# Optimization experiments

Measured on AMD Instinct MI355X. Metric: run time of the kernel, lower is better.

The kernel has to match this reference:

```python
import jax, jax.numpy as jnp
import numpy as np

N_NODES = 50000
N_EDGES = 1250000
IN_CH = 64
HID = 64
N_CLASSES = 10
N_GRAPHS = 128


def _xavier(key, shape):
    fan_out, fan_in = shape
    limit = np.sqrt(6.0 / (fan_in + fan_out))
    return jax.random.uniform(key, shape, jnp.float32, -limit, limit)


def setup_inputs() -> dict:
    key = jax.random.key(0)
    ks = jax.random.split(key, 12)
    x = jax.random.normal(ks[0], (N_NODES, IN_CH), jnp.float32)
    edge_index = jax.random.randint(ks[1], (2, N_EDGES), 0, N_NODES, jnp.int64)
    batch = jnp.sort(jax.random.randint(ks[2], (N_NODES,), 0, N_GRAPHS, jnp.int64))
    return {
        "x": x,
        "edge_index": edge_index,
        "batch": batch,
        # GraphConv i: lin_rel (weight+bias) applied to aggregated neighbors,
        # lin_root (no bias) applied to self features. Weights are [out, in].
        "W1_rel": _xavier(ks[3], (HID, IN_CH)), "b1": jnp.zeros((HID,), jnp.float32),
        "W1_root": _xavier(ks[4], (HID, IN_CH)),
        "W2_rel": _xavier(ks[5], (HID, HID)), "b2": jnp.zeros((HID,), jnp.float32),
        "W2_root": _xavier(ks[6], (HID, HID)),
        "W3_rel": _xavier(ks[7], (HID, HID)), "b3": jnp.zeros((HID,), jnp.float32),
        "W3_root": _xavier(ks[8], (HID, HID)),
        "W_lin": _xavier(ks[9], (N_CLASSES, HID)), "b_lin": jnp.zeros((N_CLASSES,), jnp.float32),
    }


def _graph_conv(x, src, dst, W_rel, b, W_root):
    # sum-aggregate neighbor features: gather at src, scatter-add at dst
    agg = jax.ops.segment_sum(x[src], dst, num_segments=N_NODES)  # [N, F]
    return agg @ W_rel.T + b + x @ W_root.T


def reference(x, edge_index, batch, W1_rel, b1, W1_root, W2_rel, b2, W2_root,
              W3_rel, b3, W3_root, W_lin, b_lin):
    src, dst = edge_index[0], edge_index[1]
    h = jax.nn.relu(_graph_conv(x, src, dst, W1_rel, b1, W1_root))
    h = jax.nn.relu(_graph_conv(h, src, dst, W2_rel, b2, W2_root))
    h = _graph_conv(h, src, dst, W3_rel, b3, W3_root)
    # global mean pool over graphs
    sums = jax.ops.segment_sum(h, batch, num_segments=N_GRAPHS)        # [G, HID]
    counts = jax.ops.segment_sum(jnp.ones((h.shape[0],), h.dtype), batch,
                                 num_segments=N_GRAPHS)
    pooled = sums / jnp.maximum(counts, 1.0)[:, None]
    out = pooled @ W_lin.T + b_lin  # dropout inactive in eval mode
    return (pooled, out)
```

## Files before the change

### kernel.cpp

```cpp
#include <hip/hip_runtime.h>

#define N_NODES   50000
#define HID       64
#define N_GRAPHS  128
#define N_CLASSES 10
#define NP        196
#define EPA       2048
#define PCAP      8192

typedef __attribute__((ext_vector_type(8))) short short8;
typedef __attribute__((ext_vector_type(4))) float f32x4;

__device__ __forceinline__ unsigned bf16rne(float f) {
    unsigned u = __float_as_uint(f);
    return (u + 0x7fffu + ((u >> 16) & 1u)) >> 16;
}
__device__ __forceinline__ unsigned pack_bf16x2(float lo, float hi) {
    return bf16rne(lo) | (bf16rne(hi) << 16);
}



__global__ void cvt_kernel(const float* __restrict__ x, unsigned short* __restrict__ xb,
                           int* __restrict__ gcursor) {
    if (blockIdx.x == 0 && threadIdx.x < NP) gcursor[threadIdx.x] = 0;
    int i = blockIdx.x * blockDim.x + threadIdx.x;
    if (i < N_NODES * 16) {
        float4 v = ((const float4*)x)[i];
        uint2 o;
        o.x = pack_bf16x2(v.x, v.y);
        o.y = pack_bf16x2(v.z, v.w);
        ((uint2*)xb)[i] = o;
    }
}


__global__ __launch_bounds__(256) void bucket_kernel(
    const int* __restrict__ src, const int* __restrict__ dst,
    int* __restrict__ gcursor, unsigned* __restrict__ packed, int E) {
    __shared__ int hist[NP], scp[NP], base[NP], cnt2[NP];
    __shared__ int sc[256];
    __shared__ unsigned stag[EPA];
    const int t = threadIdx.x;
    const int e0 = blockIdx.x * EPA;
    const int e1 = min(e0 + EPA, E);
    for (int i = t; i < NP; i += 256) { hist[i] = 0; cnt2[i] = 0; }
    __syncthreads();
    for (int e = e0 + t; e < e1; e += 256)
        atomicAdd(&hist[dst[e] >> 8], 1);
    __syncthreads();
    sc[t] = (t < NP) ? hist[t] : 0;
    __syncthreads();
    for (int off = 1; off < 256; off <<= 1) {
        int add = (t >= off) ? sc[t - off] : 0;
        __syncthreads();
        sc[t] += add;
        __syncthreads();
    }
    if (t < NP) {
        scp[t] = sc[t] - hist[t];
        if (hist[t] > 0) base[t] = atomicAdd(&gcursor[t], hist[t]);
    }
    __syncthreads();
    for (int e = e0 + t; e < e1; e += 256) {
        int d = dst[e], s = src[e];
        int p = d >> 8;
        int idx = scp[p] + atomicAdd(&cnt2[p], 1);
        stag[idx] = (unsigned)s | ((unsigned)(d & 255) << 16) | ((unsigned)p << 24);
    }
    __syncthreads();
    const int n = e1 - e0;
    for (int i = t; i < n; i += 256) {
        unsigned v = stag[i];
        int p = v >> 24;
        packed[(size_t)p * PCAP + base[p] + (i - scp[p])] = v & 0x00FFFFFFu;
    }
}

__global__ __launch_bounds__(256) void build_kernel(
    const unsigned* __restrict__ packed, const int* __restrict__ gcursor,
    int* __restrict__ offsets, unsigned short* __restrict__ csr,
    int* __restrict__ sums_zero) {
    __shared__ int hist[256], lofs[256], cnt[256], sc[256], gv[256];
    __shared__ unsigned short lcsr[PCAP];
    const int p = blockIdx.x, t = threadIdx.x;

    if (p == 0) {
        for (int i = t; i < N_GRAPHS * 64 + N_GRAPHS; i += 256) sums_zero[i] = 0;
    }

    int v = (t < NP) ? gcursor[t] : 0;
    sc[t] = v; gv[t] = v;
    __syncthreads();
    for (int off = 1; off < 256; off <<= 1) {
        int add = (t >= off) ? sc[t - off] : 0;
        __syncthreads();
        sc[t] += add;
        __syncthreads();
    }
    const int pb = sc[p] - gv[p];
    const int ne = gv[p];
    if (p == NP - 1 && t == 0) offsets[N_NODES] = sc[NP - 1];
    __syncthreads();

    const unsigned* mypk = packed + (size_t)p * PCAP;
    hist[t] = 0; cnt[t] = 0;
    __syncthreads();
    for (int i = t; i < ne; i += 256)
        atomicAdd(&hist[(mypk[i] >> 16) & 255], 1);
    __syncthreads();
    sc[t] = hist[t];
    __syncthreads();
    for (int off = 1; off < 256; off <<= 1) {
        int add = (t >= off) ? sc[t - off] : 0;
        __syncthreads();
        sc[t] += add;
        __syncthreads();
    }
    lofs[t] = sc[t] - hist[t];
    int node = p * 256 + t;
    if (node < N_NODES) offsets[node] = pb + lofs[t];
    __syncthreads();
    for (int i = t; i < ne; i += 256) {
        unsigned vv = mypk[i];
        int dl = (vv >> 16) & 255;
        int slot = lofs[dl] + atomicAdd(&cnt[dl], 1);
        lcsr[slot] = (unsigned short)(vv & 0xFFFFu);
    }
    __syncthreads();
    for (int i = t; i < ne; i += 256) csr[pb + i] = lcsr[i];
}


__global__ __launch_bounds__(256) void gather_kernel(
    const unsigned short* __restrict__ hin,
    const int* __restrict__ offsets, const unsigned short* __restrict__ csr_src,
    unsigned short* __restrict__ agg) {
    const int w = threadIdx.x >> 6, lane = threadIdx.x & 63;
    const int rg = lane >> 3;
    const int cg = lane & 7;
    const int n = blockIdx.x * 4 + w;
    const int beg = offsets[n], end = offsets[n + 1];

    float acc[8] = {0.f, 0.f, 0.f, 0.f, 0.f, 0.f, 0.f, 0.f};
    for (int base = beg; base < end; base += 64) {
        int cnt = min(64, end - base);
        int sidx = (base + lane < end) ? (int)csr_src[base + lane] : 0;
        for (int kb = 0; kb < cnt; kb += 32) {
            uint4 u[4];
#pragma unroll
            for (int p = 0; p < 4; ++p) {
                int e = kb + 8 * p + rg;
                int r = __shfl(sidx, e);
                if (e < cnt)
                    u[p] = *((const uint4*)(hin + (size_t)r * 64) + cg);
                else
                    u[p] = make_uint4(0u, 0u, 0u, 0u);
            }
#pragma unroll
            for (int p = 0; p < 4; ++p) {
                acc[0] += __uint_as_float(u[p].x << 16);
                acc[1] += __uint_as_float(u[p].x & 0xffff0000u);
                acc[2] += __uint_as_float(u[p].y << 16);
                acc[3] += __uint_as_float(u[p].y & 0xffff0000u);
                acc[4] += __uint_as_float(u[p].z << 16);
                acc[5] += __uint_as_float(u[p].z & 0xffff0000u);
                acc[6] += __uint_as_float(u[p].w << 16);
                acc[7] += __uint_as_float(u[p].w & 0xffff0000u);
            }
        }
    }
#pragma unroll
    for (int m = 8; m <= 32; m <<= 1)
#pragma unroll
        for (int j = 0; j < 8; ++j)
            acc[j] += __shfl_xor(acc[j], m);
    if (rg == 0) {
        uint4 o;
        o.x = pack_bf16x2(acc[0], acc[1]);
        o.y = pack_bf16x2(acc[2], acc[3]);
        o.z = pack_bf16x2(acc[4], acc[5]);
        o.w = pack_bf16x2(acc[6], acc[7]);
        *((uint4*)(agg + (size_t)n * 64) + cg) = o;
    }
}


template <int RELU>
__global__ __launch_bounds__(256) void linear_kernel(
    const unsigned short* __restrict__ agg,
    const unsigned short* __restrict__ hin,
    const float* __restrict__ Wrel, const float* __restrict__ bias,
    const float* __restrict__ Wroot, unsigned short* __restrict__ hout) {
    __shared__ unsigned short outT[4][16][72];

    const int tid = threadIdx.x;
    const int w = tid >> 6, lane = tid & 63;
    const int q = lane >> 4, c = lane & 15;
    const int g0 = (blockIdx.x * 4 + w) * 16;
    if (g0 >= N_NODES) return;

    short8 brel[4][2], broot[4][2];
    float biasv[4];
#pragma unroll
    for (int t = 0; t < 4; ++t) {
        int o = t * 16 + c;
        biasv[t] = bias[o];
#pragma unroll
        for (int s = 0; s < 2; ++s) {
            const float4* pr = (const float4*)(Wrel  + o * 64 + s * 32 + q * 8);
            const float4* po = (const float4*)(Wroot + o * 64 + s * 32 + q * 8);
            float4 r0 = pr[0], r1 = pr[1], z0 = po[0], z1 = po[1];
            short8 rr, zz;
            rr[0] = (short)bf16rne(r0.x); rr[1] = (short)bf16rne(r0.y);
            rr[2] = (short)bf16rne(r0.z); rr[3] = (short)bf16rne(r0.w);
            rr[4] = (short)bf16rne(r1.x); rr[5] = (short)bf16rne(r1.y);
            rr[6] = (short)bf16rne(r1.z); rr[7] = (short)bf16rne(r1.w);
            zz[0] = (short)bf16rne(z0.x); zz[1] = (short)bf16rne(z0.y);
            zz[2] = (short)bf16rne(z0.z); zz[3] = (short)bf16rne(z0.w);
            zz[4] = (short)bf16rne(z1.x); zz[5] = (short)bf16rne(z1.y);
            zz[6] = (short)bf16rne(z1.z); zz[7] = (short)bf16rne(z1.w);
            brel[t][s] = rr; broot[t][s] = zz;
        }
    }

    const int na = min(g0 + c, N_NODES - 1);
    short8 a_agg[2], a_x[2];
#pragma unroll
    for (int s = 0; s < 2; ++s) {
        a_agg[s] = *(const short8*)(agg + (size_t)na * 64 + s * 32 + q * 8);
        a_x[s]   = *(const short8*)(hin + (size_t)na * 64 + s * 32 + q * 8);
    }

    f32x4 acc4[4];
#pragma unroll
    for (int t = 0; t < 4; ++t) {
        f32x4 a0 = {biasv[t], biasv[t], biasv[t], biasv[t]};
        a0 = __builtin_amdgcn_mfma_f32_16x16x32_bf16(a_agg[0], brel[t][0], a0, 0, 0, 0);
        a0 = __builtin_amdgcn_mfma_f32_16x16x32_bf16(a_agg[1], brel[t][1], a0, 0, 0, 0);
        a0 = __builtin_amdgcn_mfma_f32_16x16x32_bf16(a_x[0],  broot[t][0], a0, 0, 0, 0);
        a0 = __builtin_amdgcn_mfma_f32_16x16x32_bf16(a_x[1],  broot[t][1], a0, 0, 0, 0);
        acc4[t] = a0;
    }

#pragma unroll
    for (int t = 0; t < 4; ++t)
#pragma unroll
        for (int r = 0; r < 4; ++r) {
            float v = acc4[t][r];
            if (RELU) v = fmaxf(v, 0.f);
            outT[w][q * 4 + r][t * 16 + c] = (unsigned short)bf16rne(v);
        }

#pragma unroll
    for (int it = 0; it < 2; ++it) {
        int row = it * 8 + (lane >> 3);
        int ch = (lane & 7) * 8;
        int n = g0 + row;
        if (n < N_NODES) {
            short8 v = *(const short8*)&outT[w][row][ch];
            *(short8*)(hout + (size_t)n * 64 + ch) = v;
        }
    }
}


__global__ __launch_bounds__(256) void pool_kernel(
    const unsigned short* __restrict__ h, const int* __restrict__ batch,
    float* __restrict__ sums, int* __restrict__ cnt) {
    int tid = threadIdx.x;
    int w = tid >> 6, lane = tid & 63;
    int n0 = blockIdx.x * 128 + w * 32;
    if (n0 >= N_NODES) return;
    int nend = min(n0 + 32, N_NODES);
    int cur = batch[n0];
    float acc = 0.f;
    int run = 0;
    for (int n = n0; n < nend; ++n) {
        int g = batch[n];
        if (g != cur) {
            atomicAdd(&sums[cur * 64 + lane], acc);
            if (lane == 0) atomicAdd(&cnt[cur], run);
            acc = 0.f; run = 0; cur = g;
        }
        unsigned u = h[(size_t)n * 64 + lane];
        acc += __uint_as_float(u << 16);
        run++;
    }
    atomicAdd(&sums[cur * 64 + lane], acc);
    if (lane == 0) atomicAdd(&cnt[cur], run);
}

__global__ void final_kernel(const float* __restrict__ sums, const int* __restrict__ cnt,
                             const float* __restrict__ Wlin, const float* __restrict__ blin,
                             float* __restrict__ out) {
    __shared__ float pl[64];
    int g = blockIdx.x, lane = threadIdx.x;
    float cdiv = fmaxf((float)cnt[g], 1.0f);
    float p = sums[g * 64 + lane] / cdiv;
    out[g * 64 + lane] = p;
    pl[lane] = p;
    __syncthreads();
    if (lane < N_CLASSES) {
        float o = blin[lane];
#pragma unroll
        for (int k = 0; k < 64; ++k) o += pl[k] * Wlin[lane * 64 + k];
        out[N_GRAPHS * 64 + g * N_CLASSES + lane] = o;
    }
}


extern "C" void kernel_launch(void* const* d_in, const int* in_sizes, int n_in,
                              void* d_out, int out_size, void* d_ws, size_t ws_size,
                              hipStream_t stream) {
    const float* x     = (const float*)d_in[0];
    const int*   ei    = (const int*)d_in[1];
    const int*   batch = (const int*)d_in[2];
    const float* W1r = (const float*)d_in[3];
    const float* b1  = (const float*)d_in[4];
    const float* W1o = (const float*)d_in[5];
    const float* W2r = (const float*)d_in[6];
    const float* b2  = (const float*)d_in[7];
    const float* W2o = (const float*)d_in[8];
    const float* W3r = (const float*)d_in[9];
    const float* b3  = (const float*)d_in[10];
    const float* W3o = (const float*)d_in[11];
    const float* Wl  = (const float*)d_in[12];
    const float* bl  = (const float*)d_in[13];
    float* out = (float*)d_out;

    const int E = in_sizes[1] / 2;
    const int* src = ei;
    const int* dst = ei + E;

    char* p = (char*)d_ws;
    unsigned short* xb  = (unsigned short*)p; p += (size_t)N_NODES * 64 * 2;
    unsigned short* h1  = (unsigned short*)p; p += (size_t)N_NODES * 64 * 2;
    unsigned short* h2  = (unsigned short*)p; p += (size_t)N_NODES * 64 * 2;
    unsigned short* agg = (unsigned short*)p; p += (size_t)N_NODES * 64 * 2;
    unsigned short* h3  = h1;
    unsigned* packed    = (unsigned*)p; p += (size_t)NP * PCAP * 4;
    unsigned short* csr = (unsigned short*)p; p += (size_t)E * 2;
    int* offsets   = (int*)p;   p += (size_t)(N_NODES + 1) * 4;
    int* gcursor   = (int*)p;   p += NP * 4;
    float* sums    = (float*)p; p += (size_t)N_GRAPHS * 64 * 4;
    int* cnt       = (int*)p;   p += N_GRAPHS * 4;

    const int NCHUNK = (E + EPA - 1) / EPA;
    cvt_kernel<<<(N_NODES * 16 + 255) / 256, 256, 0, stream>>>(x, xb, gcursor);
    bucket_kernel<<<NCHUNK, 256, 0, stream>>>(src, dst, gcursor, packed, E);
    build_kernel<<<NP, 256, 0, stream>>>(packed, gcursor, offsets, csr, (int*)sums);

    const int GB = N_NODES / 4;
    const int LB = (N_NODES + 63) / 64;
    gather_kernel<<<GB, 256, 0, stream>>>(xb, offsets, csr, agg);
    linear_kernel<1><<<LB, 256, 0, stream>>>(agg, xb, W1r, b1, W1o, h1);
    gather_kernel<<<GB, 256, 0, stream>>>(h1, offsets, csr, agg);
    linear_kernel<1><<<LB, 256, 0, stream>>>(agg, h1, W2r, b2, W2o, h2);
    gather_kernel<<<GB, 256, 0, stream>>>(h2, offsets, csr, agg);
    linear_kernel<0><<<LB, 256, 0, stream>>>(agg, h2, W3r, b3, W3o, h3);

    pool_kernel<<<(N_NODES + 127) / 128, 256, 0, stream>>>(h3, batch, sums, cnt);
    final_kernel<<<N_GRAPHS, 64, 0, stream>>>(sums, cnt, Wl, bl, out);
}
```

Measured before the change: 271.5 us.

## Replace two-level bucketed CSR build with global atomic count/scan/scatter

Swaps the bucket-then-local-sort CSR construction for a simpler pipeline: per-node degree counting with global atomics, a per-block scan to produce offsets and cursors, then a scatter using a global atomic on each destination's cursor. It drops the large packed staging buffer and the shared-memory local sort, but adds two full passes of global atomics over the edges. Edge order within each node becomes nondeterministic, so the order of floating-point sums in the gather can vary from run to run.

```diff
diff --git a/kernel.cpp b/kernel.cpp
--- a/kernel.cpp
+++ b/kernel.cpp
@@ -5,8 +5,7 @@
 #define N_GRAPHS  128
 #define N_CLASSES 10
 #define NP        196
-#define EPA       2048
-#define PCAP      8192
+#define NPAD      50176
 
 typedef __attribute__((ext_vector_type(8))) short short8;
 typedef __attribute__((ext_vector_type(4))) float f32x4;
@@ -20,11 +19,12 @@
 }
 
 
+#define NZERO (NPAD + N_GRAPHS * 64 + N_GRAPHS)
 
 __global__ void cvt_kernel(const float* __restrict__ x, unsigned short* __restrict__ xb,
-                           int* __restrict__ gcursor) {
-    if (blockIdx.x == 0 && threadIdx.x < NP) gcursor[threadIdx.x] = 0;
+                           int* __restrict__ zspan) {
     int i = blockIdx.x * blockDim.x + threadIdx.x;
+    if (i < NZERO) zspan[i] = 0;
     if (i < N_NODES * 16) {
         float4 v = ((const float4*)x)[i];
         uint2 o;
@@ -35,21 +35,32 @@
 }
 
 
-__global__ __launch_bounds__(256) void bucket_kernel(
-    const int* __restrict__ src, const int* __restrict__ dst,
-    int* __restrict__ gcursor, unsigned* __restrict__ packed, int E) {
-    __shared__ int hist[NP], scp[NP], base[NP], cnt2[NP];
+__global__ __launch_bounds__(256) void count_kernel(
+    const int* __restrict__ dst, int* __restrict__ deg, int E) {
+    int e = blockIdx.x * 256 + threadIdx.x;
+    if (e < E) atomicAdd(&deg[dst[e]], 1);
+}
+
+__global__ __launch_bounds__(256) void offsets_kernel(
+    const int* __restrict__ deg, int* __restrict__ offsets,
+    int* __restrict__ cursor) {
+    __shared__ int part[256];
     __shared__ int sc[256];
-    __shared__ unsigned stag[EPA];
-    const int t = threadIdx.x;
-    const int e0 = blockIdx.x * EPA;
-    const int e1 = min(e0 + EPA, E);
-    for (int i = t; i < NP; i += 256) { hist[i] = 0; cnt2[i] = 0; }
-    __syncthreads();
-    for (int e = e0 + t; e < e1; e += 256)
-        atomicAdd(&hist[dst[e] >> 8], 1);
-    __syncthreads();
-    sc[t] = (t < NP) ? hist[t] : 0;
+    const int p = blockIdx.x, t = threadIdx.x;
+    const int w = t >> 6, lane = t & 63;
+
+    for (int c = w; c < NP; c += 4) {
+        int base = c * 256;
+        int s = deg[base + lane] + deg[base + 64 + lane]
+              + deg[base + 128 + lane] + deg[base + 192 + lane];
+#pragma unroll
+        for (int m = 1; m < 64; m <<= 1) s += __shfl_xor(s, m);
+        if (lane == 0) part[c] = s;
+    }
+    if (t >= NP) part[t] = 0;
+    __syncthreads();
+
+    sc[t] = part[t];
     __syncthreads();
     for (int off = 1; off < 256; off <<= 1) {
         int add = (t >= off) ? sc[t - off] : 0;
@@ -57,40 +68,12 @@
         sc[t] += add;
         __syncthreads();
     }
-    if (t < NP) {
-        scp[t] = sc[t] - hist[t];
-        if (hist[t] > 0) base[t] = atomicAdd(&gcursor[t], hist[t]);
-    }
-    __syncthreads();
-    for (int e = e0 + t; e < e1; e += 256) {
-        int d = dst[e], s = src[e];
-        int p = d >> 8;
-        int idx = scp[p] + atomicAdd(&cnt2[p], 1);
-        stag[idx] = (unsigned)s | ((unsigned)(d & 255) << 16) | ((unsigned)p << 24);
-    }
-    __syncthreads();
-    const int n = e1 - e0;
-    for (int i = t; i < n; i += 256) {
-        unsigned v = stag[i];
-        int p = v >> 24;
-        packed[(size_t)p * PCAP + base[p] + (i - scp[p])] = v & 0x00FFFFFFu;
-    }
-}
-
-__global__ __launch_bounds__(256) void build_kernel(
-    const unsigned* __restrict__ packed, const int* __restrict__ gcursor,
-    int* __restrict__ offsets, unsigned short* __restrict__ csr,
-    int* __restrict__ sums_zero) {
-    __shared__ int hist[256], lofs[256], cnt[256], sc[256], gv[256];
-    __shared__ unsigned short lcsr[PCAP];
-    const int p = blockIdx.x, t = threadIdx.x;
-
-    if (p == 0) {
-        for (int i = t; i < N_GRAPHS * 64 + N_GRAPHS; i += 256) sums_zero[i] = 0;
-    }
-
-    int v = (t < NP) ? gcursor[t] : 0;
-    sc[t] = v; gv[t] = v;
+    const int pbase = sc[p] - part[p];
+    __syncthreads();
+
+    const int node = p * 256 + t;
+    const int d = (node < N_NODES) ? deg[node] : 0;
+    sc[t] = d;
     __syncthreads();
     for (int off = 1; off < 256; off <<= 1) {
         int add = (t >= off) ? sc[t - off] : 0;
@@ -98,37 +81,21 @@
         sc[t] += add;
         __syncthreads();
     }
-    const int pb = sc[p] - gv[p];
-    const int ne = gv[p];
-    if (p == NP - 1 && t == 0) offsets[N_NODES] = sc[NP - 1];
-    __syncthreads();
-
-    const unsigned* mypk = packed + (size_t)p * PCAP;
-    hist[t] = 0; cnt[t] = 0;
-    __syncthreads();
-    for (int i = t; i < ne; i += 256)
-        atomicAdd(&hist[(mypk[i] >> 16) & 255], 1);
-    __syncthreads();
-    sc[t] = hist[t];
-    __syncthreads();
-    for (int off = 1; off < 256; off <<= 1) {
-        int add = (t >= off) ? sc[t - off] : 0;
-        __syncthreads();
-        sc[t] += add;
-        __syncthreads();
-    }
-    lofs[t] = sc[t] - hist[t];
-    int node = p * 256 + t;
-    if (node < N_NODES) offsets[node] = pb + lofs[t];
-    __syncthreads();
-    for (int i = t; i < ne; i += 256) {
-        unsigned vv = mypk[i];
-        int dl = (vv >> 16) & 255;
-        int slot = lofs[dl] + atomicAdd(&cnt[dl], 1);
-        lcsr[slot] = (unsigned short)(vv & 0xFFFFu);
-    }
-    __syncthreads();
-    for (int i = t; i < ne; i += 256) csr[pb + i] = lcsr[i];
+    if (node <= N_NODES) {
+        int o = pbase + sc[t] - d;
+        offsets[node] = o;
+        if (node < N_NODES) cursor[node] = o;
+    }
+}
+
+__global__ __launch_bounds__(256) void scatter_kernel(
+    const int* __restrict__ src, const int* __restrict__ dst,
+    int* __restrict__ cursor, unsigned short* __restrict__ csr, int E) {
+    int e = blockIdx.x * 256 + threadIdx.x;
+    if (e < E) {
+        int pos = atomicAdd(&cursor[dst[e]], 1);
+        csr[pos] = (unsigned short)src[e];
+    }
 }
 
 
@@ -339,17 +306,18 @@
     unsigned short* h2  = (unsigned short*)p; p += (size_t)N_NODES * 64 * 2;
     unsigned short* agg = (unsigned short*)p; p += (size_t)N_NODES * 64 * 2;
     unsigned short* h3  = h1;
-    unsigned* packed    = (unsigned*)p; p += (size_t)NP * PCAP * 4;
-    unsigned short* csr = (unsigned short*)p; p += (size_t)E * 2;
-    int* offsets   = (int*)p;   p += (size_t)(N_NODES + 1) * 4;
-    int* gcursor   = (int*)p;   p += NP * 4;
+    unsigned short* csr = (unsigned short*)p; p += ((size_t)E * 2 + 255) & ~255ull;
+    int* offsets   = (int*)p;   p += (size_t)(N_NODES + 64) * 4;
+    int* deg       = (int*)p;   p += (size_t)NPAD * 4;
     float* sums    = (float*)p; p += (size_t)N_GRAPHS * 64 * 4;
     int* cnt       = (int*)p;   p += N_GRAPHS * 4;
-
-    const int NCHUNK = (E + EPA - 1) / EPA;
-    cvt_kernel<<<(N_NODES * 16 + 255) / 256, 256, 0, stream>>>(x, xb, gcursor);
-    bucket_kernel<<<NCHUNK, 256, 0, stream>>>(src, dst, gcursor, packed, E);
-    build_kernel<<<NP, 256, 0, stream>>>(packed, gcursor, offsets, csr, (int*)sums);
+    int* cursor    = (int*)p;   p += (size_t)NPAD * 4;
+
+    const int EB = (E + 255) / 256;
+    cvt_kernel<<<(N_NODES * 16 + 255) / 256, 256, 0, stream>>>(x, xb, deg);
+    count_kernel<<<EB, 256, 0, stream>>>(dst, deg, E);
+    offsets_kernel<<<NP, 256, 0, stream>>>(deg, offsets, cursor);
+    scatter_kernel<<<EB, 256, 0, stream>>>(src, dst, cursor, csr, E);
 
     const int GB = N_NODES / 4;
     const int LB = (N_NODES + 63) / 64;
```

Result: slower. 391.3 us (+44.2%).
